# Optimization experiments

Measured on AMD Instinct MI355X. Metric: run time of the kernel, lower is better.

The kernel has to match this reference:

```python
import jax, jax.numpy as jnp
import numpy as np

N_HEADS = 16
D_HEAD = 64
MAX_POS = 128

def setup_inputs() -> dict:
    key = jax.random.key(0)
    ks = jax.random.split(key, 9)
    B, L, D = 4, 1024, 1024
    s = 0.02
    return {
        'x': jax.random.normal(ks[0], (B, L, D), jnp.float32),
        'pad_mask': jnp.ones((B, L), jnp.float32),
        'Wq': jax.random.normal(ks[1], (D, D), jnp.float32) * s,
        'bq': jnp.zeros((D,), jnp.float32),
        'Wk': jax.random.normal(ks[2], (D, D), jnp.float32) * s,
        'bk': jnp.zeros((D,), jnp.float32),
        'Wv': jax.random.normal(ks[3], (D, D), jnp.float32) * s,
        'bv': jnp.zeros((D,), jnp.float32),
        'Wo': jax.random.normal(ks[4], (D, D), jnp.float32) * s,
        'bo': jnp.zeros((D,), jnp.float32),
        'posK': jax.random.normal(ks[5], (2 * MAX_POS + 1, D_HEAD), jnp.float32) * s,
        'posV': jax.random.normal(ks[6], (2 * MAX_POS + 1, D_HEAD), jnp.float32) * s,
    }

def reference(x, pad_mask, Wq, bq, Wk, bk, Wv, bv, Wo, bo, posK, posV):
    B, L, _ = x.shape
    H, d = N_HEADS, D_HEAD
    def proj(W, b):
        y = x @ W + b                      # [B, L, H*d]
        return y.reshape(B, L, H, d).transpose(0, 2, 1, 3)  # [B, H, L, d]
    Q = proj(Wq, bq)
    K = proj(Wk, bk)
    V = proj(Wv, bv)
    # relative position index, clamped to [-MAX_POS, MAX_POS], shifted to [0, 2*MAX_POS]
    idx = jnp.arange(L)
    pos_index = jnp.clip(idx[None, :] - idx[:, None], -MAX_POS, MAX_POS) + MAX_POS  # [L, L]
    pos_emb_K = posK[pos_index]            # [L, L, d]
    pos_emb_V = posV[pos_index]            # [L, L, d]
    S1 = jnp.einsum('bhqd,bhkd->bhqk', Q, K)
    S2 = jnp.einsum('bhqd,qkd->bhqk', Q, pos_emb_K)
    S = (S1 + S2) / np.sqrt(d).astype(np.float32)
    # NOTE: original multiplies scores by the pad mask (not additive -inf)
    S = S * pad_mask[:, None, None, :]
    A = jax.nn.softmax(S, axis=-1)
    O1 = jnp.einsum('bhqk,bhkd->bhqd', A, V)
    O2 = jnp.einsum('bhqk,qkd->bhqd', A, pos_emb_V)
    out = (O1 + O2).transpose(0, 2, 1, 3).reshape(B, L, H * d)
    return out @ Wo + bo
```

## Files before the change

kernel.cpp:

```cpp
#include <hip/hip_runtime.h>
#include <math.h>

#define L_SEQ 1024
#define NB 4
#define NH 16
#define DH 64
#define BH_TOT (NB * NH)
#define GQ_TOT (BH_TOT * L_SEQ)
#define NPOS 257
#define QP_STRIDE 260
#define LDK 72
#define LDQP 72
#define LDPV 264
#define LDK32 40

typedef unsigned short ushort_t;
typedef __attribute__((ext_vector_type(8))) short bf16x8;
typedef __attribute__((ext_vector_type(4))) float f32x4;

__device__ inline ushort_t f2bf_rne(float x) {
    unsigned u = __float_as_uint(x);
    unsigned r = u + 0x7FFFu + ((u >> 16) & 1u);
    return (ushort_t)(r >> 16);
}
__device__ inline float bf2f(ushort_t h) {
    return __uint_as_float(((unsigned)h) << 16);
}
__device__ inline uint4 pack8hi(float4 a0, float4 a1) {
    float v[8] = {a0.x, a0.y, a0.z, a0.w, a1.x, a1.y, a1.z, a1.w};
    unsigned hh[4];
    #pragma unroll
    for (int j = 0; j < 4; j++)
        hh[j] = (unsigned)f2bf_rne(v[2*j]) | ((unsigned)f2bf_rne(v[2*j+1]) << 16);
    return (uint4){hh[0], hh[1], hh[2], hh[3]};
}

__global__ __launch_bounds__(256)
void split_f32_hi(const float* __restrict__ A, ushort_t* __restrict__ hi)
{
    const size_t base = ((size_t)blockIdx.x * 256 + threadIdx.x) * 8;
    *(uint4*)(hi + base) =
        pack8hi(*(const float4*)(A + base), *(const float4*)(A + base + 4));
}

__global__ __launch_bounds__(256)
void split_transpose3(const float* __restrict__ Wq, const float* __restrict__ Wk,
                      const float* __restrict__ Wv, ushort_t* __restrict__ Thi,
                      ushort_t* __restrict__ Tlo)
{
    __shared__ float Ws[64][65];
    const int tid = threadIdx.x;
    const int k0 = blockIdx.x * 64;
    const int n0 = blockIdx.y * 64;
    const int z  = blockIdx.z;
    const float* W = (z == 0) ? Wq : (z == 1) ? Wk : Wv;
    ushort_t* Hh = Thi + (size_t)z * 1048576;
    ushort_t* Ll = Tlo + (size_t)z * 1048576;
    const int r  = tid >> 4;
    const int c4 = (tid & 15) * 4;
    #pragma unroll
    for (int i = 0; i < 4; i++) {
        float4 v = *(const float4*)(W + (size_t)(k0 + r + i*16) * 1024 + n0 + c4);
        Ws[r + i*16][c4+0] = v.x;
        Ws[r + i*16][c4+1] = v.y;
        Ws[r + i*16][c4+2] = v.z;
        Ws[r + i*16][c4+3] = v.w;
    }
    __syncthreads();
    #pragma unroll
    for (int i = 0; i < 4; i++) {
        const int nl = r + i*16;
        ushort_t h[4], l[4];
        #pragma unroll
        for (int j = 0; j < 4; j++) {
            float x = Ws[c4 + j][nl];
            h[j] = f2bf_rne(x);
            l[j] = f2bf_rne(x - bf2f(h[j]));
        }
        size_t off = (size_t)(n0 + nl) * 1024 + k0 + c4;
        uint2 H, L;
        H.x = (unsigned)h[0] | ((unsigned)h[1] << 16);
        H.y = (unsigned)h[2] | ((unsigned)h[3] << 16);
        L.x = (unsigned)l[0] | ((unsigned)l[1] << 16);
        L.y = (unsigned)l[2] | ((unsigned)l[3] << 16);
        *(uint2*)(Hh + off) = H;
        *(uint2*)(Ll + off) = L;
    }
}

__global__ __launch_bounds__(256)
void split_transpose(const float* __restrict__ W, ushort_t* __restrict__ Thi,
                     ushort_t* __restrict__ Tlo, int Kdim, int Ndim)
{
    __shared__ float Ws[64][65];
    const int tid = threadIdx.x;
    const int k0 = blockIdx.x * 64;
    const int n0 = blockIdx.y * 64;
    const int r  = tid >> 4;
    const int c4 = (tid & 15) * 4;
    #pragma unroll
    for (int i = 0; i < 4; i++) {
        float4 v = *(const float4*)(W + (size_t)(k0 + r + i*16) * Ndim + n0 + c4);
        Ws[r + i*16][c4+0] = v.x;
        Ws[r + i*16][c4+1] = v.y;
        Ws[r + i*16][c4+2] = v.z;
        Ws[r + i*16][c4+3] = v.w;
    }
    __syncthreads();
    #pragma unroll
    for (int i = 0; i < 4; i++) {
        const int nl = r + i*16;
        ushort_t h[4], l[4];
        #pragma unroll
        for (int j = 0; j < 4; j++) {
            float x = Ws[c4 + j][nl];
            h[j] = f2bf_rne(x);
            l[j] = f2bf_rne(x - bf2f(h[j]));
        }
        size_t off = (size_t)(n0 + nl) * Kdim + k0 + c4;
        uint2 H, L;
        H.x = (unsigned)h[0] | ((unsigned)h[1] << 16);
        H.y = (unsigned)h[2] | ((unsigned)h[3] << 16);
        L.x = (unsigned)l[0] | ((unsigned)l[1] << 16);
        L.y = (unsigned)l[2] | ((unsigned)l[3] << 16);
        *(uint2*)(Thi + off) = H;
        *(uint2*)(Tlo + off) = L;
    }
}

__global__ __launch_bounds__(256)
void prep_pvt(const float* __restrict__ posV, ushort_t* __restrict__ pvTg)
{
    __shared__ float Ws[64][65];
    const int tid = threadIdx.x;
    const int c = blockIdx.x;
    {
        const int r  = tid >> 2;
        const int d0 = (tid & 3) * 16;
        const float* src = posV + (size_t)(c * 64 + r + 1) * 64 + d0;
        #pragma unroll
        for (int i = 0; i < 4; i++) {
            float4 v = *(const float4*)(src + i * 4);
            Ws[r][d0 + i*4 + 0] = v.x;
            Ws[r][d0 + i*4 + 1] = v.y;
            Ws[r][d0 + i*4 + 2] = v.z;
            Ws[r][d0 + i*4 + 3] = v.w;
        }
    }
    __syncthreads();
    {
        const int d  = tid >> 2;
        const int r0 = (tid & 3) * 16;
        #pragma unroll
        for (int k = 0; k < 16; k++)
            pvTg[(size_t)d * LDPV + c * 64 + r0 + k] = f2bf_rne(Ws[r0 + k][d]);
    }
}

__global__ __launch_bounds__(256)
void gemm_qkv128(const ushort_t* __restrict__ Ahi,
                 const ushort_t* __restrict__ Bhi, const ushort_t* __restrict__ Blo,
                 const float* __restrict__ bq, const float* __restrict__ bk,
                 const float* __restrict__ bv,
                 ushort_t* __restrict__ Qbu, ushort_t* __restrict__ Kbu,
                 ushort_t* __restrict__ Vtu)
{
    __shared__ ushort_t As[128 * LDK32];
    __shared__ ushort_t Bs[2][128 * LDK32];
    const int tid  = threadIdx.x;
    const int m0   = blockIdx.x * 128;
    const int n0   = blockIdx.y * 128;
    const int nb   = n0 >> 10;
    const int wave = tid >> 6, lane = tid & 63;
    const int wr = wave >> 1, wc = wave & 1;
    const int lr = lane & 15, lq = lane >> 4;
    const int K = 1024;

    const int r0 = tid >> 1,        c0 = (tid & 1) * 16;
    const int sA0 = tid,       rA0 = sA0 >> 2, cA0 = (sA0 & 3) * 8;
    const int sA1 = 256 + tid, rA1 = sA1 >> 2, cA1 = (sA1 & 3) * 8;
    (void)r0; (void)c0;

    f32x4 acc[4][4];
    #pragma unroll
    for (int i = 0; i < 4; i++)
        #pragma unroll
        for (int j = 0; j < 4; j++)
            acc[i][j] = (f32x4){0.f, 0.f, 0.f, 0.f};

    uint4 pa0, pa1, pbh0, pbh1, pbl0, pbl1;
    {
        const size_t a0 = (size_t)(m0 + rA0) * K + cA0, a1 = (size_t)(m0 + rA1) * K + cA1;
        const size_t b0 = (size_t)(n0 + rA0) * K + cA0, b1 = (size_t)(n0 + rA1) * K + cA1;
        pa0  = *(const uint4*)(Ahi + a0); pa1  = *(const uint4*)(Ahi + a1);
        pbh0 = *(const uint4*)(Bhi + b0); pbh1 = *(const uint4*)(Bhi + b1);
        pbl0 = *(const uint4*)(Blo + b0); pbl1 = *(const uint4*)(Blo + b1);
    }

    for (int it = 0; it < 32; it++) {
        __syncthreads();
        *(uint4*)&As[rA0 * LDK32 + cA0]    = pa0;
        *(uint4*)&As[rA1 * LDK32 + cA1]    = pa1;
        *(uint4*)&Bs[0][rA0 * LDK32 + cA0] = pbh0;
        *(uint4*)&Bs[0][rA1 * LDK32 + cA1] = pbh1;
        *(uint4*)&Bs[1][rA0 * LDK32 + cA0] = pbl0;
        *(uint4*)&Bs[1][rA1 * LDK32 + cA1] = pbl1;
        __syncthreads();
        if (it < 31) {
            const int k0 = (it + 1) * 32;
            const size_t a0 = (size_t)(m0 + rA0) * K + k0 + cA0, a1 = (size_t)(m0 + rA1) * K + k0 + cA1;
            const size_t b0 = (size_t)(n0 + rA0) * K + k0 + cA0, b1 = (size_t)(n0 + rA1) * K + k0 + cA1;
            pa0  = *(const uint4*)(Ahi + a0); pa1  = *(const uint4*)(Ahi + a1);
            pbh0 = *(const uint4*)(Bhi + b0); pbh1 = *(const uint4*)(Bhi + b1);
            pbl0 = *(const uint4*)(Blo + b0); pbl1 = *(const uint4*)(Blo + b1);
        }

        bf16x8 ah[4], bh[4], bl[4];
        #pragma unroll
        for (int i = 0; i < 4; i++) {
            ah[i] = *(const bf16x8*)&As[(wr*64 + i*16 + lr) * LDK32 + lq*8];
            const int br = (wc*64 + i*16 + lr) * LDK32 + lq*8;
            bh[i] = *(const bf16x8*)&Bs[0][br];
            bl[i] = *(const bf16x8*)&Bs[1][br];
        }
        #pragma unroll
        for (int i = 0; i < 4; i++)
            #pragma unroll
            for (int j = 0; j < 4; j++) {
                acc[i][j] = __builtin_amdgcn_mfma_f32_16x16x32_bf16(ah[i], bh[j], acc[i][j], 0, 0, 0);
                acc[i][j] = __builtin_amdgcn_mfma_f32_16x16x32_bf16(ah[i], bl[j], acc[i][j], 0, 0, 0);
            }
    }

    const float* bp = (nb == 0) ? bq : (nb == 1) ? bk : bv;
    ushort_t* Cout = (nb == 0) ? Qbu : (nb == 1) ? Kbu : Vtu;
    #pragma unroll
    for (int j = 0; j < 4; j++) {
        const int colg = n0 + wc*64 + j*16 + lr;
        const int c1   = colg & 1023;
        const float bcol = bp[c1];
        const int h = c1 >> 6, dd = c1 & 63;
        #pragma unroll
        for (int i = 0; i < 4; i++) {
            #pragma unroll
            for (int r = 0; r < 4; r++) {
                const int m = m0 + wr*64 + i*16 + lq*4 + r;
                const float v = acc[i][j][r] + bcol;
                const int b = m >> 10, lp = m & 1023;
                const size_t off = (nb == 2)
                    ? ((size_t)(b * NH + h) * DH + dd) * L_SEQ + lp
                    : ((size_t)(b * NH + h) * L_SEQ + lp) * DH + dd;
                Cout[off] = f2bf_rne(v);
            }
        }
    }
}

__global__ __launch_bounds__(256)
void gemm_mfma(const ushort_t* __restrict__ Ahi, const ushort_t* __restrict__ Alo,
               const ushort_t* __restrict__ Bhi, const ushort_t* __restrict__ Blo,
               const float* __restrict__ bias, float* __restrict__ C,
               int M, int N, int K)
{
    __shared__ ushort_t As[2][64 * LDK];
    __shared__ ushort_t Bs[2][64 * LDK];
    const int tid  = threadIdx.x;
    const int m0   = blockIdx.x * 64;
    const int n0   = blockIdx.y * 64;
    const int wave = tid >> 6, lane = tid & 63;
    const int w0 = wave >> 1, w1 = wave & 1;
    const int lr = lane & 15, lq = lane >> 4;

    f32x4 acc[2][2];
    #pragma unroll
    for (int i = 0; i < 2; i++)
        #pragma unroll
        for (int j = 0; j < 2; j++)
            acc[i][j] = (f32x4){0.f, 0.f, 0.f, 0.f};

    for (int k0 = 0; k0 < K; k0 += 64) {
        __syncthreads();
        #pragma unroll
        for (int c = 0; c < 2; c++) {
            const int n   = c * 256 + tid;
            const int row = n >> 3;
            const int col = (n & 7) * 8;
            const size_t ga = (size_t)(m0 + row) * K + k0 + col;
            const size_t gb = (size_t)(n0 + row) * K + k0 + col;
            const int la = row * LDK + col;
            *(uint4*)&As[0][la] = *(const uint4*)(Ahi + ga);
            *(uint4*)&As[1][la] = *(const uint4*)(Alo + ga);
            *(uint4*)&Bs[0][la] = *(const uint4*)(Bhi + gb);
            *(uint4*)&Bs[1][la] = *(const uint4*)(Blo + gb);
        }
        __syncthreads();
        #pragma unroll
        for (int ks = 0; ks < 2; ks++) {
            bf16x8 ah[2], al[2], bh[2], bl[2];
            #pragma unroll
            for (int i = 0; i < 2; i++) {
                const int ar = (w0*32 + i*16 + lr) * LDK + ks*32 + lq*8;
                ah[i] = *(const bf16x8*)&As[0][ar];
                al[i] = *(const bf16x8*)&As[1][ar];
                const int br = (w1*32 + i*16 + lr) * LDK + ks*32 + lq*8;
                bh[i] = *(const bf16x8*)&Bs[0][br];
                bl[i] = *(const bf16x8*)&Bs[1][br];
            }
            #pragma unroll
            for (int i = 0; i < 2; i++)
                #pragma unroll
                for (int j = 0; j < 2; j++) {
                    acc[i][j] = __builtin_amdgcn_mfma_f32_16x16x32_bf16(ah[i], bh[j], acc[i][j], 0, 0, 0);
                    acc[i][j] = __builtin_amdgcn_mfma_f32_16x16x32_bf16(ah[i], bl[j], acc[i][j], 0, 0, 0);
                    acc[i][j] = __builtin_amdgcn_mfma_f32_16x16x32_bf16(al[i], bh[j], acc[i][j], 0, 0, 0);
                }
        }
    }

    #pragma unroll
    for (int j = 0; j < 2; j++) {
        const int colg = n0 + w1*32 + j*16 + lr;
        const float bcol = bias[colg];
        #pragma unroll
        for (int i = 0; i < 2; i++) {
            #pragma unroll
            for (int r = 0; r < 4; r++) {
                const int m = m0 + w0*32 + i*16 + lq*4 + r;
                C[(size_t)m * N + colg] = acc[i][j][r] + bcol;
            }
        }
    }
}

__global__ __launch_bounds__(256)
void qp_mfma(const ushort_t* __restrict__ Qu, const float* __restrict__ posK,
             ushort_t* __restrict__ Qpu)
{
    const int tid = threadIdx.x;
    const size_t m0 = (size_t)blockIdx.x * 64;
    const int n0 = blockIdx.y * 64;
    const int wave = tid >> 6, lane = tid & 63;
    const int wm = (wave >> 1) * 32, wn = (wave & 1) * 32;
    const int lr = lane & 15, lq = lane >> 4;

    bf16x8 af[2][2];
    #pragma unroll
    for (int i = 0; i < 2; i++) {
        const ushort_t* qrow = Qu + (m0 + wm + i*16 + lr) * DH;
        #pragma unroll
        for (int kc = 0; kc < 2; kc++)
            af[i][kc] = *(const bf16x8*)(qrow + kc*32 + lq*8);
    }
    bf16x8 bf[2][2];
    #pragma unroll
    for (int j = 0; j < 2; j++) {
        int n = n0 + wn + j*16 + lr;
        const float* krow = posK + (size_t)(n < 256 ? n : 256) * DH;
        #pragma unroll
        for (int kc = 0; kc < 2; kc++) {
            const float* s = krow + kc*32 + lq*8;
            uint4 u = pack8hi(*(const float4*)s, *(const float4*)(s + 4));
            bf[j][kc] = *(bf16x8*)&u;
        }
    }

    f32x4 acc[2][2];
    #pragma unroll
    for (int i = 0; i < 2; i++)
        #pragma unroll
        for (int j = 0; j < 2; j++)
            acc[i][j] = (f32x4){0.f, 0.f, 0.f, 0.f};
    #pragma unroll
    for (int kc = 0; kc < 2; kc++)
        #pragma unroll
        for (int i = 0; i < 2; i++)
            #pragma unroll
            for (int j = 0; j < 2; j++)
                acc[i][j] = __builtin_amdgcn_mfma_f32_16x16x32_bf16(af[i][kc], bf[j][kc], acc[i][j], 0, 0, 0);

    #pragma unroll
    for (int i = 0; i < 2; i++)
        #pragma unroll
        for (int j = 0; j < 2; j++) {
            const int n = n0 + wn + j*16 + lr;
            if (n < NPOS) {
                #pragma unroll
                for (int r = 0; r < 4; r++) {
                    const size_t m = m0 + wm + i*16 + lq*4 + r;
                    Qpu[m * QP_STRIDE + n] = f2bf_rne(acc[i][j][r]);
                }
            }
        }
}

__global__ __launch_bounds__(256)
void attn_kernel(const ushort_t* __restrict__ Qu, const ushort_t* __restrict__ Ku,
                 const ushort_t* __restrict__ Vtu, const ushort_t* __restrict__ Qpu,
                 const float* __restrict__ pm,
                 ushort_t* __restrict__ SbandU,
                 ushort_t* __restrict__ O1a, ushort_t* __restrict__ O1b,
                 float* __restrict__ lsum2, float* __restrict__ clo2,
                 float* __restrict__ chi2)
{
    __shared__ ushort_t Ks[64 * LDK];
    __shared__ ushort_t Vs[64 * LDK];
    __shared__ ushort_t QpsP[64 * LDQP];
    __shared__ float mk[64];

    const int tid = threadIdx.x;
    const int blk = blockIdx.x;
    const int bh  = blk >> 5;
    const int qb  = (blk >> 1) & 15;
    const int ks  = blk & 1;
    const int b   = bh >> 4;
    const int q0  = qb * 64;
    const size_t gq0 = (size_t)bh * L_SEQ + q0;
    const int wave = tid >> 6, lane = tid & 63;
    const int lr = lane & 15, lq = lane >> 4;
    const int qw = wave * 16;

    const int sr0 = tid >> 3,          sc0 = (tid & 7) * 8;
    const int sr1 = (256 + tid) >> 3,  sc1 = ((256 + tid) & 7) * 8;
    const int qpRowL = qw + (lane >> 2);
    const int qpCol0 = (lane & 3) * 16;

    const ushort_t* Kg  = Ku  + (size_t)bh * (L_SEQ * DH);
    const ushort_t* Vtg = Vtu + (size_t)bh * (DH * L_SEQ);

    bf16x8 qa[2];
    {
        const ushort_t* qrow = Qu + (gq0 + qw + lr) * DH;
        #pragma unroll
        for (int kc = 0; kc < 2; kc++)
            qa[kc] = *(const bf16x8*)(qrow + kc * 32 + lq * 8);
    }

    if (ks == 0 && tid < 64) {
        const int q = q0 + tid;
        ushort_t* bandRow = SbandU + (gq0 + tid) * 256;
        for (int j = 0; j < 127 - q; j++)    bandRow[j] = 0;
        for (int j = 254; j > 1150 - q; j--) bandRow[j] = 0;
        bandRow[255] = 0;
    }

    f32x4 Oacc[4];
    #pragma unroll
    for (int j = 0; j < 4; j++) Oacc[j] = (f32x4){0.f, 0.f, 0.f, 0.f};
    float lpart[4] = {}, clpart[4] = {}, chpart[4] = {};

    uint4 kva0, kva1, kvb0, kvb1;
    ushort_t qpr[16];
    float mkr = 0.f;
    {
        const int k0 = ks * 512;
        kva0 = *(const uint4*)(Kg + (size_t)(k0 + sr0) * DH + sc0);
        kva1 = *(const uint4*)(Kg + (size_t)(k0 + sr1) * DH + sc1);
        kvb0 = *(const uint4*)(Vtg + (size_t)sr0 * L_SEQ + k0 + sc0);
        kvb1 = *(const uint4*)(Vtg + (size_t)sr1 * L_SEQ + k0 + sc1);
        const int qg = q0 + qpRowL;
        #pragma unroll
        for (int c = 0; c < 16; c++) {
            int rel = k0 + qpCol0 + c - qg;
            rel = rel < -128 ? -128 : (rel > 128 ? 128 : rel);
            qpr[c] = Qpu[(gq0 + qpRowL) * QP_STRIDE + rel + 128];
        }
        if (tid < 64) mkr = pm[b * L_SEQ + k0 + tid];
    }

    for (int t = 0; t < 8; t++) {
        const int k0 = (ks * 8 + t) * 64;
        __syncthreads();

        *(uint4*)&Ks[sr0 * LDK + sc0] = kva0;
        *(uint4*)&Ks[sr1 * LDK + sc1] = kva1;
        *(uint4*)&Vs[sr0 * LDK + sc0] = kvb0;
        *(uint4*)&Vs[sr1 * LDK + sc1] = kvb1;
        {
            ushort_t* dst = &QpsP[qpRowL * LDQP + qpCol0];
            #pragma unroll
            for (int c = 0; c < 8; c++)
                ((unsigned*)dst)[c] = (unsigned)qpr[2*c] | ((unsigned)qpr[2*c+1] << 16);
        }
        if (tid < 64) mk[tid] = mkr;
        __syncthreads();

        if (t < 7) {
            const int k0n = k0 + 64;
            kva0 = *(const uint4*)(Kg + (size_t)(k0n + sr0) * DH + sc0);
            kva1 = *(const uint4*)(Kg + (size_t)(k0n + sr1) * DH + sc1);
            kvb0 = *(const uint4*)(Vtg + (size_t)sr0 * L_SEQ + k0n + sc0);
            kvb1 = *(const uint4*)(Vtg + (size_t)sr1 * L_SEQ + k0n + sc1);
            const int qg = q0 + qpRowL;
            #pragma unroll
            for (int c = 0; c < 16; c++) {
                int rel = k0n + qpCol0 + c - qg;
                rel = rel < -128 ? -128 : (rel > 128 ? 128 : rel);
                qpr[c] = Qpu[(gq0 + qpRowL) * QP_STRIDE + rel + 128];
            }
            if (tid < 64) mkr = pm[b * L_SEQ + k0n + tid];
        }

        f32x4 Sacc[4];
        #pragma unroll
        for (int j = 0; j < 4; j++) Sacc[j] = (f32x4){0.f, 0.f, 0.f, 0.f};
        #pragma unroll
        for (int kc = 0; kc < 2; kc++) {
            #pragma unroll
            for (int j = 0; j < 4; j++) {
                bf16x8 kb = *(const bf16x8*)&Ks[(j*16 + lr) * LDK + kc*32 + lq*8];
                Sacc[j] = __builtin_amdgcn_mfma_f32_16x16x32_bf16(qa[kc], kb, Sacc[j], 0, 0, 0);
            }
        }

        ushort_t pb[4][4];
        #pragma unroll
        for (int r = 0; r < 4; r++) {
            const int ql = qw + lq*4 + r;
            const int q  = q0 + ql;
            const size_t gq = gq0 + ql;
            ushort_t* bandRow = SbandU + gq * 256 + 127;
            #pragma unroll
            for (int j = 0; j < 4; j++) {
                const int kl = j*16 + lr;
                const int k  = k0 + kl;
                const int rel = k - q;
                float s = (Sacc[j][r] + bf2f(QpsP[ql * LDQP + kl])) * 0.125f;
                s *= mk[kl];
                const float p = __expf(s);
                lpart[r] += p;
                const ushort_t ph = f2bf_rne(p);
                if (rel <= -128)      clpart[r] += p;
                else if (rel >= 128)  chpart[r] += p;
                else                  bandRow[rel] = ph;
                pb[j][r] = ph;
            }
        }

        #pragma unroll
        for (int r = 0; r < 4; r++)
            #pragma unroll
            for (int j = 0; j < 4; j++)
                QpsP[(qw + lq*4 + r) * LDQP + j*16 + lr] = pb[j][r];

        #pragma unroll
        for (int kc = 0; kc < 2; kc++) {
            bf16x8 pa = *(const bf16x8*)&QpsP[(qw + lr) * LDQP + kc*32 + lq*8];
            #pragma unroll
            for (int j = 0; j < 4; j++) {
                bf16x8 vb = *(const bf16x8*)&Vs[(j*16 + lr) * LDK + kc*32 + lq*8];
                Oacc[j] = __builtin_amdgcn_mfma_f32_16x16x32_bf16(pa, vb, Oacc[j], 0, 0, 0);
            }
        }
    }

    #pragma unroll
    for (int off = 1; off < 16; off <<= 1) {
        #pragma unroll
        for (int r = 0; r < 4; r++) {
            lpart[r]  += __shfl_xor(lpart[r],  off, 64);
            clpart[r] += __shfl_xor(clpart[r], off, 64);
            chpart[r] += __shfl_xor(chpart[r], off, 64);
        }
    }
    if (lr == 0) {
        #pragma unroll
        for (int r = 0; r < 4; r++) {
            const size_t o = (size_t)ks * GQ_TOT + gq0 + qw + lq*4 + r;
            lsum2[o] = lpart[r];
            clo2[o]  = clpart[r];
            chi2[o]  = chpart[r];
        }
    }

    ushort_t* O1o = ks ? O1b : O1a;
    #pragma unroll
    for (int j = 0; j < 4; j++)
        #pragma unroll
        for (int r = 0; r < 4; r++)
            O1o[(gq0 + qw + lq*4 + r) * DH + j*16 + lr] = f2bf_rne(Oacc[j][r]);
}

__global__ __launch_bounds__(256)
void post_mfma(const ushort_t* __restrict__ SbandU, const ushort_t* __restrict__ pvTg,
               const ushort_t* __restrict__ O1a, const ushort_t* __restrict__ O1b,
               const float* __restrict__ lsum2, const float* __restrict__ clo2,
               const float* __restrict__ chi2, const float* __restrict__ posV,
               ushort_t* __restrict__ athi, ushort_t* __restrict__ atlo)
{
    __shared__ ushort_t pvT[64 * LDPV];
    const int tid = threadIdx.x;
    const size_t q0 = (size_t)blockIdx.x * 64;
    const int wave = tid >> 6, lane = tid & 63;
    const int w0 = wave >> 1, w1 = wave & 1;
    const int lr = lane & 15, lq = lane >> 4;

    {
        const unsigned* src = (const unsigned*)pvTg;
        unsigned* dst = (unsigned*)pvT;
        for (int i = tid; i < 64 * LDPV / 2; i += 256) dst[i] = src[i];
    }
    __syncthreads();

    f32x4 acc[2][2];
    #pragma unroll
    for (int i = 0; i < 2; i++)
        #pragma unroll
        for (int j = 0; j < 2; j++)
            acc[i][j] = (f32x4){0.f, 0.f, 0.f, 0.f};

    const ushort_t* bandB = SbandU + q0 * 256;
    #pragma unroll
    for (int kc = 0; kc < 8; kc++) {
        bf16x8 a[2], bv[2];
        #pragma unroll
        for (int i = 0; i < 2; i++) {
            a[i]  = *(const bf16x8*)&bandB[(size_t)(w0*32 + i*16 + lr) * 256 + kc*32 + lq*8];
            bv[i] = *(const bf16x8*)&pvT[(w1*32 + i*16 + lr) * LDPV + kc*32 + lq*8];
        }
        #pragma unroll
        for (int i = 0; i < 2; i++)
            #pragma unroll
            for (int j = 0; j < 2; j++)
                acc[i][j] = __builtin_amdgcn_mfma_f32_16x16x32_bf16(a[i], bv[j], acc[i][j], 0, 0, 0);
    }

    #pragma unroll
    for (int i = 0; i < 2; i++) {
        #pragma unroll
        for (int r = 0; r < 4; r++) {
            const int ql = w0*32 + i*16 + lq*4 + r;
            const size_t gq = q0 + ql;
            const float li = lsum2[gq] + lsum2[GQ_TOT + gq];
            const float cl = clo2[gq]  + clo2[GQ_TOT + gq];
            const float ch = chi2[gq]  + chi2[GQ_TOT + gq];
            const float inv = 1.0f / li;
            const int b  = (int)(gq >> 14);
            const int h  = (int)((gq >> 10) & 15);
            const int lp = (int)(gq & 1023);
            const size_t obase = ((size_t)(b * L_SEQ + lp) * 1024) + h * 64;
            #pragma unroll
            for (int j = 0; j < 2; j++) {
                const int dd = w1*32 + j*16 + lr;
                float o = bf2f(O1a[gq * DH + dd]) + bf2f(O1b[gq * DH + dd])
                        + acc[i][j][r]
                        + cl * posV[dd] + ch * posV[256 * 64 + dd];
                o *= inv;
                const ushort_t hh = f2bf_rne(o);
                const ushort_t ll = f2bf_rne(o - bf2f(hh));
                athi[obase + dd] = hh;
                atlo[obase + dd] = ll;
            }
        }
    }
}

extern "C" void kernel_launch(void* const* d_in, const int* in_sizes, int n_in,
                              void* d_out, int out_size, void* d_ws, size_t ws_size,
                              hipStream_t stream)
{
    const float* x    = (const float*)d_in[0];
    const float* pmk  = (const float*)d_in[1];
    const float* Wq   = (const float*)d_in[2];
    const float* bq   = (const float*)d_in[3];
    const float* Wk   = (const float*)d_in[4];
    const float* bk   = (const float*)d_in[5];
    const float* Wv   = (const float*)d_in[6];
    const float* bv   = (const float*)d_in[7];
    const float* Wo   = (const float*)d_in[8];
    const float* bo   = (const float*)d_in[9];
    const float* posK = (const float*)d_in[10];
    const float* posV = (const float*)d_in[11];
    float* out = (float*)d_out;

    ushort_t* u = (ushort_t*)d_ws;
    ushort_t* Qbu    = u;
    ushort_t* Kbu    = Qbu + (size_t)GQ_TOT * DH;
    ushort_t* Vtu    = Kbu + (size_t)GQ_TOT * DH;
    ushort_t* Qpu    = Vtu + (size_t)GQ_TOT * DH;
    ushort_t* SbandU = Qpu + (size_t)GQ_TOT * QP_STRIDE;
    ushort_t* athi   = SbandU + (size_t)GQ_TOT * 256;
    ushort_t* atlo   = athi + (size_t)GQ_TOT * DH;
    ushort_t* O1a    = atlo + (size_t)GQ_TOT * DH;
    ushort_t* O1b    = O1a  + (size_t)GQ_TOT * DH;
    ushort_t* pvTg   = O1b  + (size_t)GQ_TOT * DH;
    float* lsum2 = (float*)(pvTg + 64 * LDPV + 64);
    float* clo2  = lsum2 + 2 * (size_t)GQ_TOT;
    float* chi2  = clo2  + 2 * (size_t)GQ_TOT;

    ushort_t* bb    = SbandU;
    ushort_t* xhi   = bb;
    ushort_t* wqkvh = xhi + 4194304;
    ushort_t* wqkvl = wqkvh + 3145728;
    ushort_t* woh   = bb;
    ushort_t* wol   = woh + 1048576;

    dim3 gb(256);

    split_f32_hi<<<dim3(2048), gb, 0, stream>>>(x, xhi);
    split_transpose3<<<dim3(16, 16, 3), gb, 0, stream>>>(Wq, Wk, Wv, wqkvh, wqkvl);
    prep_pvt<<<dim3(4), gb, 0, stream>>>(posV, pvTg);
    gemm_qkv128<<<dim3(32, 24), gb, 0, stream>>>(xhi, wqkvh, wqkvl, bq, bk, bv,
                                                 Qbu, Kbu, Vtu);
    qp_mfma<<<dim3(1024, 5), gb, 0, stream>>>(Qbu, posK, Qpu);
    attn_kernel<<<dim3(2048), gb, 0, stream>>>(Qbu, Kbu, Vtu, Qpu, pmk,
                                               SbandU, O1a, O1b, lsum2, clo2, chi2);
    post_mfma<<<dim3(GQ_TOT / 64), gb, 0, stream>>>(SbandU, pvTg, O1a, O1b, lsum2,
                                                    clo2, chi2, posV, athi, atlo);
    split_transpose<<<dim3(16, 16), gb, 0, stream>>>(Wo, woh, wol, 1024, 1024);
    gemm_mfma<<<dim3(64, 16), gb, 0, stream>>>(athi, atlo, woh, wol, bo, out,
                                               4096, 1024, 1024);
}
```

Before: 359.9 us.

## Use 128x128 register-prefetched tiles for output GEMM and coalesce Qp gather

Replaces the 64x64-tile output projection GEMM with a 128x128-tile kernel. It uses a 4x4 MFMA accumulator per wave and prefetches the next K-slice into registers while computing the current one. This raises data reuse per LDS load and hides global load latency, but launches only 256 blocks, which may underfill the device. Separately, the attention kernel's relative-position Qp gather is remapped so that lanes read consecutive key columns of one query row, making the global reads coalesced, at the cost of 16 scalar 16-bit LDS stores instead of 8 packed ones.

```diff
diff --git a/kernel.cpp b/kernel.cpp
--- a/kernel.cpp
+++ b/kernel.cpp
@@ -176,10 +176,8 @@
     const int lr = lane & 15, lq = lane >> 4;
     const int K = 1024;
 
-    const int r0 = tid >> 1,        c0 = (tid & 1) * 16;
     const int sA0 = tid,       rA0 = sA0 >> 2, cA0 = (sA0 & 3) * 8;
     const int sA1 = 256 + tid, rA1 = sA1 >> 2, cA1 = (sA1 & 3) * 8;
-    (void)r0; (void)c0;
 
     f32x4 acc[4][4];
     #pragma unroll
@@ -257,75 +255,90 @@
 }
 
 __global__ __launch_bounds__(256)
-void gemm_mfma(const ushort_t* __restrict__ Ahi, const ushort_t* __restrict__ Alo,
-               const ushort_t* __restrict__ Bhi, const ushort_t* __restrict__ Blo,
-               const float* __restrict__ bias, float* __restrict__ C,
-               int M, int N, int K)
-{
-    __shared__ ushort_t As[2][64 * LDK];
-    __shared__ ushort_t Bs[2][64 * LDK];
+void gemm_out128(const ushort_t* __restrict__ Ahi, const ushort_t* __restrict__ Alo,
+                 const ushort_t* __restrict__ Bhi, const ushort_t* __restrict__ Blo,
+                 const float* __restrict__ bias, float* __restrict__ C)
+{
+    __shared__ ushort_t As[2][128 * LDK32];
+    __shared__ ushort_t Bs[2][128 * LDK32];
     const int tid  = threadIdx.x;
-    const int m0   = blockIdx.x * 64;
-    const int n0   = blockIdx.y * 64;
+    const int m0   = blockIdx.x * 128;
+    const int n0   = blockIdx.y * 128;
     const int wave = tid >> 6, lane = tid & 63;
-    const int w0 = wave >> 1, w1 = wave & 1;
+    const int wr = wave >> 1, wc = wave & 1;
     const int lr = lane & 15, lq = lane >> 4;
-
-    f32x4 acc[2][2];
-    #pragma unroll
-    for (int i = 0; i < 2; i++)
-        #pragma unroll
-        for (int j = 0; j < 2; j++)
+    const int K = 1024, N = 1024;
+
+    const int sA0 = tid,       rA0 = sA0 >> 2, cA0 = (sA0 & 3) * 8;
+    const int sA1 = 256 + tid, rA1 = sA1 >> 2, cA1 = (sA1 & 3) * 8;
+
+    f32x4 acc[4][4];
+    #pragma unroll
+    for (int i = 0; i < 4; i++)
+        #pragma unroll
+        for (int j = 0; j < 4; j++)
             acc[i][j] = (f32x4){0.f, 0.f, 0.f, 0.f};
 
-    for (int k0 = 0; k0 < K; k0 += 64) {
+    uint4 pah0, pah1, pal0, pal1, pbh0, pbh1, pbl0, pbl1;
+    {
+        const size_t a0 = (size_t)(m0 + rA0) * K + cA0, a1 = (size_t)(m0 + rA1) * K + cA1;
+        const size_t b0 = (size_t)(n0 + rA0) * K + cA0, b1 = (size_t)(n0 + rA1) * K + cA1;
+        pah0 = *(const uint4*)(Ahi + a0); pah1 = *(const uint4*)(Ahi + a1);
+        pal0 = *(const uint4*)(Alo + a0); pal1 = *(const uint4*)(Alo + a1);
+        pbh0 = *(const uint4*)(Bhi + b0); pbh1 = *(const uint4*)(Bhi + b1);
+        pbl0 = *(const uint4*)(Blo + b0); pbl1 = *(const uint4*)(Blo + b1);
+    }
+
+    for (int it = 0; it < 32; it++) {
         __syncthreads();
-        #pragma unroll
-        for (int c = 0; c < 2; c++) {
-            const int n   = c * 256 + tid;
-            const int row = n >> 3;
-            const int col = (n & 7) * 8;
-            const size_t ga = (size_t)(m0 + row) * K + k0 + col;
-            const size_t gb = (size_t)(n0 + row) * K + k0 + col;
-            const int la = row * LDK + col;
-            *(uint4*)&As[0][la] = *(const uint4*)(Ahi + ga);
-            *(uint4*)&As[1][la] = *(const uint4*)(Alo + ga);
-            *(uint4*)&Bs[0][la] = *(const uint4*)(Bhi + gb);
-            *(uint4*)&Bs[1][la] = *(const uint4*)(Blo + gb);
-        }
+        *(uint4*)&As[0][rA0 * LDK32 + cA0] = pah0;
+        *(uint4*)&As[0][rA1 * LDK32 + cA1] = pah1;
+        *(uint4*)&As[1][rA0 * LDK32 + cA0] = pal0;
+        *(uint4*)&As[1][rA1 * LDK32 + cA1] = pal1;
+        *(uint4*)&Bs[0][rA0 * LDK32 + cA0] = pbh0;
+        *(uint4*)&Bs[0][rA1 * LDK32 + cA1] = pbh1;
+        *(uint4*)&Bs[1][rA0 * LDK32 + cA0] = pbl0;
+        *(uint4*)&Bs[1][rA1 * LDK32 + cA1] = pbl1;
         __syncthreads();
-        #pragma unroll
-        for (int ks = 0; ks < 2; ks++) {
-            bf16x8 ah[2], al[2], bh[2], bl[2];
-            #pragma unroll
-            for (int i = 0; i < 2; i++) {
-                const int ar = (w0*32 + i*16 + lr) * LDK + ks*32 + lq*8;
-                ah[i] = *(const bf16x8*)&As[0][ar];
-                al[i] = *(const bf16x8*)&As[1][ar];
-                const int br = (w1*32 + i*16 + lr) * LDK + ks*32 + lq*8;
-                bh[i] = *(const bf16x8*)&Bs[0][br];
-                bl[i] = *(const bf16x8*)&Bs[1][br];
-            }
-            #pragma unroll
-            for (int i = 0; i < 2; i++)
-                #pragma unroll
-                for (int j = 0; j < 2; j++) {
-                    acc[i][j] = __builtin_amdgcn_mfma_f32_16x16x32_bf16(ah[i], bh[j], acc[i][j], 0, 0, 0);
-                    acc[i][j] = __builtin_amdgcn_mfma_f32_16x16x32_bf16(ah[i], bl[j], acc[i][j], 0, 0, 0);
-                    acc[i][j] = __builtin_amdgcn_mfma_f32_16x16x32_bf16(al[i], bh[j], acc[i][j], 0, 0, 0);
-                }
-        }
-    }
-
-    #pragma unroll
-    for (int j = 0; j < 2; j++) {
-        const int colg = n0 + w1*32 + j*16 + lr;
+        if (it < 31) {
+            const int k0 = (it + 1) * 32;
+            const size_t a0 = (size_t)(m0 + rA0) * K + k0 + cA0, a1 = (size_t)(m0 + rA1) * K + k0 + cA1;
+            const size_t b0 = (size_t)(n0 + rA0) * K + k0 + cA0, b1 = (size_t)(n0 + rA1) * K + k0 + cA1;
+            pah0 = *(const uint4*)(Ahi + a0); pah1 = *(const uint4*)(Ahi + a1);
+            pal0 = *(const uint4*)(Alo + a0); pal1 = *(const uint4*)(Alo + a1);
+            pbh0 = *(const uint4*)(Bhi + b0); pbh1 = *(const uint4*)(Bhi + b1);
+            pbl0 = *(const uint4*)(Blo + b0); pbl1 = *(const uint4*)(Blo + b1);
+        }
+
+        bf16x8 ah[4], al[4], bh[4], bl[4];
+        #pragma unroll
+        for (int i = 0; i < 4; i++) {
+            const int ar = (wr*64 + i*16 + lr) * LDK32 + lq*8;
+            ah[i] = *(const bf16x8*)&As[0][ar];
+            al[i] = *(const bf16x8*)&As[1][ar];
+            const int br = (wc*64 + i*16 + lr) * LDK32 + lq*8;
+            bh[i] = *(const bf16x8*)&Bs[0][br];
+            bl[i] = *(const bf16x8*)&Bs[1][br];
+        }
+        #pragma unroll
+        for (int i = 0; i < 4; i++)
+            #pragma unroll
+            for (int j = 0; j < 4; j++) {
+                acc[i][j] = __builtin_amdgcn_mfma_f32_16x16x32_bf16(ah[i], bh[j], acc[i][j], 0, 0, 0);
+                acc[i][j] = __builtin_amdgcn_mfma_f32_16x16x32_bf16(ah[i], bl[j], acc[i][j], 0, 0, 0);
+                acc[i][j] = __builtin_amdgcn_mfma_f32_16x16x32_bf16(al[i], bh[j], acc[i][j], 0, 0, 0);
+            }
+    }
+
+    #pragma unroll
+    for (int j = 0; j < 4; j++) {
+        const int colg = n0 + wc*64 + j*16 + lr;
         const float bcol = bias[colg];
         #pragma unroll
-        for (int i = 0; i < 2; i++) {
+        for (int i = 0; i < 4; i++) {
             #pragma unroll
             for (int r = 0; r < 4; r++) {
-                const int m = m0 + w0*32 + i*16 + lq*4 + r;
+                const int m = m0 + wr*64 + i*16 + lq*4 + r;
                 C[(size_t)m * N + colg] = acc[i][j][r] + bcol;
             }
         }
@@ -421,8 +434,6 @@
 
     const int sr0 = tid >> 3,          sc0 = (tid & 7) * 8;
     const int sr1 = (256 + tid) >> 3,  sc1 = ((256 + tid) & 7) * 8;
-    const int qpRowL = qw + (lane >> 2);
-    const int qpCol0 = (lane & 3) * 16;
 
     const ushort_t* Kg  = Ku  + (size_t)bh * (L_SEQ * DH);
     const ushort_t* Vtg = Vtu + (size_t)bh * (DH * L_SEQ);
@@ -457,12 +468,12 @@
         kva1 = *(const uint4*)(Kg + (size_t)(k0 + sr1) * DH + sc1);
         kvb0 = *(const uint4*)(Vtg + (size_t)sr0 * L_SEQ + k0 + sc0);
         kvb1 = *(const uint4*)(Vtg + (size_t)sr1 * L_SEQ + k0 + sc1);
-        const int qg = q0 + qpRowL;
         #pragma unroll
         for (int c = 0; c < 16; c++) {
-            int rel = k0 + qpCol0 + c - qg;
+            const int ql = 4*c + wave;
+            int rel = k0 + lane - q0 - ql;
             rel = rel < -128 ? -128 : (rel > 128 ? 128 : rel);
-            qpr[c] = Qpu[(gq0 + qpRowL) * QP_STRIDE + rel + 128];
+            qpr[c] = Qpu[(gq0 + ql) * QP_STRIDE + rel + 128];
         }
         if (tid < 64) mkr = pm[b * L_SEQ + k0 + tid];
     }
@@ -475,12 +486,9 @@
         *(uint4*)&Ks[sr1 * LDK + sc1] = kva1;
         *(uint4*)&Vs[sr0 * LDK + sc0] = kvb0;
         *(uint4*)&Vs[sr1 * LDK + sc1] = kvb1;
-        {
-            ushort_t* dst = &QpsP[qpRowL * LDQP + qpCol0];
-            #pragma unroll
-            for (int c = 0; c < 8; c++)
-                ((unsigned*)dst)[c] = (unsigned)qpr[2*c] | ((unsigned)qpr[2*c+1] << 16);
-        }
+        #pragma unroll
+        for (int c = 0; c < 16; c++)
+            QpsP[(4*c + wave) * LDQP + lane] = qpr[c];
         if (tid < 64) mk[tid] = mkr;
         __syncthreads();
 
@@ -490,12 +498,12 @@
             kva1 = *(const uint4*)(Kg + (size_t)(k0n + sr1) * DH + sc1);
             kvb0 = *(const uint4*)(Vtg + (size_t)sr0 * L_SEQ + k0n + sc0);
             kvb1 = *(const uint4*)(Vtg + (size_t)sr1 * L_SEQ + k0n + sc1);
-            const int qg = q0 + qpRowL;
             #pragma unroll
             for (int c = 0; c < 16; c++) {
-                int rel = k0n + qpCol0 + c - qg;
+                const int ql = 4*c + wave;
+                int rel = k0n + lane - q0 - ql;
                 rel = rel < -128 ? -128 : (rel > 128 ? 128 : rel);
-                qpr[c] = Qpu[(gq0 + qpRowL) * QP_STRIDE + rel + 128];
+                qpr[c] = Qpu[(gq0 + ql) * QP_STRIDE + rel + 128];
             }
             if (tid < 64) mkr = pm[b * L_SEQ + k0n + tid];
         }
@@ -707,6 +715,5 @@
     post_mfma<<<dim3(GQ_TOT / 64), gb, 0, stream>>>(SbandU, pvTg, O1a, O1b, lsum2,
                                                     clo2, chi2, posV, athi, atlo);
     split_transpose<<<dim3(16, 16), gb, 0, stream>>>(Wo, woh, wol, 1024, 1024);
-    gemm_mfma<<<dim3(64, 16), gb, 0, stream>>>(athi, atlo, woh, wol, bo, out,
-                                               4096, 1024, 1024);
-}
+    gemm_out128<<<dim3(32, 8), gb, 0, stream>>>(athi, atlo, woh, wol, bo, out);
+}
```

New measurement: 363.8 us. No clear change (+1.1%).
